# Optimization experiments

Hardware: AMD Instinct MI355X
Metric: run time of the kernel (lower is better)

Reference implementation:

```python
import jax, jax.numpy as jnp
import numpy as np

N, E, L, H, C, F, NCLASS, NGRAPH = 50000, 800000, 3, 2, 64, 128, 10, 64
NEG_SLOPE = 0.2


def setup_inputs() -> dict:
    key = jax.random.key(0)
    ks = jax.random.split(key, 8)
    x = jax.random.normal(ks[0], (N, F), dtype=jnp.float32)
    edge_index = jax.random.randint(ks[1], (2, E), 0, N, dtype=jnp.int64)
    batch = jnp.sort(jax.random.randint(ks[2], (N,), 0, NGRAPH, dtype=jnp.int64))
    s = 1.0 / np.sqrt(F)
    W = jax.random.normal(ks[3], (L, F, H * C), dtype=jnp.float32) * s
    att_src = jax.random.normal(ks[4], (L, H, C), dtype=jnp.float32) * s
    att_dst = jax.random.normal(ks[5], (L, H, C), dtype=jnp.float32) * s
    bias = jnp.zeros((L, H * C), dtype=jnp.float32)
    lin_w = jax.random.normal(ks[6], (H * C, NCLASS), dtype=jnp.float32) * s
    lin_b = jnp.zeros((NCLASS,), dtype=jnp.float32)
    return {"x": x, "edge_index": edge_index, "batch": batch, "W": W,
            "att_src": att_src, "att_dst": att_dst, "bias": bias,
            "lin_w": lin_w, "lin_b": lin_b}


def _gat_layer(x, src, dst, w, a_s, a_d, b):
    n = x.shape[0]
    h = (x @ w).reshape(n, H, C)                      # [N,H,C]
    alpha_src = jnp.sum(h * a_s, axis=-1)             # [N,H]
    alpha_dst = jnp.sum(h * a_d, axis=-1)             # [N,H]
    e = jax.nn.leaky_relu(alpha_src[src] + alpha_dst[dst], NEG_SLOPE)  # [E2,H]
    # scatter-softmax over incoming edges of each destination node
    m = jax.ops.segment_max(e, dst, num_segments=n)
    p = jnp.exp(e - m[dst])
    z = jax.ops.segment_sum(p, dst, num_segments=n)
    alpha = p / z[dst]                                # [E2,H]
    msg = h[src] * alpha[:, :, None]                  # [E2,H,C]
    out = jax.ops.segment_sum(msg, dst, num_segments=n)  # [N,H,C]
    return out.reshape(n, H * C) + b


def reference(x, edge_index, batch, W, att_src, att_dst, bias, lin_w, lin_b):
    n = x.shape[0]
    # PyG GATConv default: add self-loops
    loop = jnp.arange(n, dtype=edge_index.dtype)
    src = jnp.concatenate([edge_index[0], loop])
    dst = jnp.concatenate([edge_index[1], loop])
    for l in range(L):
        x = _gat_layer(x, src, dst, W[l], att_src[l], att_dst[l], bias[l])
        x = jax.nn.elu(x)  # activation; dropout/bn inactive (eval, use_bn=False)
    # global mean pool per graph
    sums = jax.ops.segment_sum(x, batch, num_segments=NGRAPH)
    cnt = jax.ops.segment_sum(jnp.ones((n,), x.dtype), batch, num_segments=NGRAPH)
    pooled = sums / jnp.maximum(cnt, 1.0)[:, None]    # [NGRAPH, H*C]
    logits = pooled @ lin_w + lin_b
    return jax.nn.softmax(logits, axis=1)
```

## Files before the change

### kernel.cpp

```cpp
#include <hip/hip_runtime.h>
#include <math.h>

#define NNODES 50000
#define NEDGES 800000
#define NLAYERS 3
#define NHEADS 2
#define NCH 64
#define FDIM 128
#define NCLS 10
#define NGRAPH 64
#define NEG_SLOPE 0.2f
#define NBLK ((NNODES + 255) / 256)
#define GEMMB ((NNODES + 63) / 64)
#define HISTB ((NEDGES + 255) / 256)

#define WAVE_SYNC()                      \
  do {                                   \
    __builtin_amdgcn_wave_barrier();     \
    __asm__ volatile("" ::: "memory");   \
  } while (0)

typedef __attribute__((ext_vector_type(8))) short bf16x8;
typedef __attribute__((ext_vector_type(4))) float f32x4;

__device__ __forceinline__ unsigned short f2bf(float f) {
  unsigned int u = __builtin_bit_cast(unsigned int, f);
  unsigned int r = u + 0x7FFFu + ((u >> 16) & 1u);
  return (unsigned short)(r >> 16);
}
__device__ __forceinline__ float bflo(unsigned v) {
  return __builtin_bit_cast(float, v << 16);
}
__device__ __forceinline__ float bfhi(unsigned v) {
  return __builtin_bit_cast(float, v & 0xFFFF0000u);
}

__global__ __launch_bounds__(256) void k_wprep(const float* __restrict__ W,
                                               unsigned* __restrict__ Wt) {
  __shared__ float Lt[128][132];
  int l = blockIdx.x;
  const float* Wl = W + (size_t)l * FDIM * FDIM;
  unsigned* Wtl = Wt + (size_t)l * FDIM * FDIM / 2;
  int t = threadIdx.x;
#pragma unroll
  for (int i = 0; i < 16; ++i) {
    int k = (t >> 5) + 8 * i;
    int n4 = (t & 31) * 4;
    float4 v = *(const float4*)(Wl + (size_t)k * 128 + n4);
    Lt[k][n4 + 0] = v.x;
    Lt[k][n4 + 1] = v.y;
    Lt[k][n4 + 2] = v.z;
    Lt[k][n4 + 3] = v.w;
  }
  __syncthreads();
  int n = t >> 1;
  int kh = (t & 1) * 64;
  for (int kk = 0; kk < 64; kk += 2) {
    unsigned pk = (unsigned)f2bf(Lt[kh + kk][n]) |
                  ((unsigned)f2bf(Lt[kh + kk + 1][n]) << 16);
    Wtl[n * 64 + (kh >> 1) + (kk >> 1)] = pk;
  }
}


__global__ __launch_bounds__(256) void k_scan1(const int* __restrict__ deg,
                                               int* __restrict__ pre,
                                               int* __restrict__ bsum) {
  __shared__ int ps[256];
  int t = threadIdx.x;
  int i = blockIdx.x * 256 + t;
  int c = (i < NNODES) ? (deg[i] + 1) : 0;
  ps[t] = c;
  __syncthreads();
  for (int off = 1; off < 256; off <<= 1) {
    int v = (t >= off) ? ps[t - off] : 0;
    __syncthreads();
    ps[t] += v;
    __syncthreads();
  }
  if (i < NNODES) pre[i] = ps[t] - c;
  if (t == 255) bsum[blockIdx.x] = ps[255];
}

__global__ __launch_bounds__(256) void k_scan2(const int* __restrict__ bsum,
                                               int* __restrict__ boff) {
  __shared__ int ps[256];
  int t = threadIdx.x;
  int c = (t < NBLK) ? bsum[t] : 0;
  ps[t] = c;
  __syncthreads();
  for (int off = 1; off < 256; off <<= 1) {
    int v = (t >= off) ? ps[t - off] : 0;
    __syncthreads();
    ps[t] += v;
    __syncthreads();
  }
  if (t < NBLK) boff[t] = ps[t] - c;
}

__global__ void k_scan3(const int* __restrict__ pre,
                        const int* __restrict__ boff,
                        int* __restrict__ row_ptr, int* __restrict__ csr) {
  int i = blockIdx.x * 256 + threadIdx.x;
  if (i < NNODES) {
    int o = pre[i] + boff[i >> 8];
    row_ptr[i] = o;
    csr[o] = i;
  }
  if (i == 0) row_ptr[NNODES] = NEDGES + NNODES;
}

__global__ void k_scatter(const int* __restrict__ ei,
                          const int* __restrict__ row_ptr,
                          const int* __restrict__ rank, int* __restrict__ csr) {
  int e = blockIdx.x * 256 + threadIdx.x;
  if (e < NEDGES) {
    int d = ei[NEDGES + e];
    csr[row_ptr[d] + 1 + rank[e]] = ei[e];
  }
}

__device__ __forceinline__ void gemm_body(int blk, const float* __restrict__ X,
                                          const unsigned* __restrict__ Wt,
                                          const float* __restrict__ a_sL,
                                          const float* __restrict__ a_dL,
                                          unsigned* __restrict__ Hb,
                                          float* __restrict__ as_,
                                          float* __restrict__ ad_) {
  __shared__ unsigned short Xs[64][136];
  __shared__ unsigned short Wsh[128][136];
  int t = threadIdx.x;
  int lane = t & 63;
  int w = t >> 6;
  int row0 = blk * 64;

  {
    int r = t >> 2;
    int gr = row0 + r;
    const float* xp = X + (size_t)gr * 128;
#pragma unroll
    for (int i = 0; i < 8; ++i) {
      int c4 = ((t & 3) + 4 * i) * 4;
      float4 v = make_float4(0.f, 0.f, 0.f, 0.f);
      if (gr < NNODES) v = *(const float4*)(xp + c4);
      unsigned lo = (unsigned)f2bf(v.x) | ((unsigned)f2bf(v.y) << 16);
      unsigned hi = (unsigned)f2bf(v.z) | ((unsigned)f2bf(v.w) << 16);
      *(uint2*)&Xs[r][c4] = make_uint2(lo, hi);
    }
  }
  {
    int n = t >> 1;
    const uint4* wp = (const uint4*)(Wt + n * 64 + (t & 1) * 32);
    int kh = (t & 1) * 64;
#pragma unroll
    for (int i = 0; i < 8; ++i) {
      uint4 v = wp[i];
      *(uint4*)&Wsh[n][kh + i * 8] = v;
    }
  }
  __syncthreads();

  int n16 = lane & 15;
  int quad = lane >> 4;
  int m0 = w * 16;
  f32x4 acc[8];
#pragma unroll
  for (int nt = 0; nt < 8; ++nt) {
    f32x4 z = {0.f, 0.f, 0.f, 0.f};
    acc[nt] = z;
  }
#pragma unroll
  for (int kk = 0; kk < 4; ++kk) {
    bf16x8 af = *(const bf16x8*)&Xs[m0 + n16][kk * 32 + quad * 8];
#pragma unroll
    for (int nt = 0; nt < 8; ++nt) {
      bf16x8 bf = *(const bf16x8*)&Wsh[nt * 16 + n16][kk * 32 + quad * 8];
      acc[nt] =
          __builtin_amdgcn_mfma_f32_16x16x32_bf16(af, bf, acc[nt], 0, 0, 0);
    }
  }

  float asv[8], adv[8];
#pragma unroll
  for (int nt = 0; nt < 8; ++nt) {
    asv[nt] = a_sL[nt * 16 + n16];
    adv[nt] = a_dL[nt * 16 + n16];
  }
#pragma unroll
  for (int r = 0; r < 4; ++r) {
    int row = row0 + m0 + quad * 4 + r;
    bool ok = (row < NNODES);
    float ps0 = 0.f, pd0 = 0.f, ps1 = 0.f, pd1 = 0.f;
#pragma unroll
    for (int nt = 0; nt < 4; ++nt) {
      ps0 += acc[nt][r] * asv[nt];
      pd0 += acc[nt][r] * adv[nt];
      ps1 += acc[nt + 4][r] * asv[nt + 4];
      pd1 += acc[nt + 4][r] * adv[nt + 4];
    }
#pragma unroll
    for (int off = 1; off < 16; off <<= 1) {
      ps0 += __shfl_xor(ps0, off, 64);
      pd0 += __shfl_xor(pd0, off, 64);
      ps1 += __shfl_xor(ps1, off, 64);
      pd1 += __shfl_xor(pd1, off, 64);
    }
    if (ok && n16 == 0) {
      as_[row * 2 + 0] = ps0;
      as_[row * 2 + 1] = ps1;
      ad_[row * 2 + 0] = pd0;
      ad_[row * 2 + 1] = pd1;
    }
    if (ok) {
#pragma unroll
      for (int nt = 0; nt < 4; ++nt) {
        unsigned pk = (unsigned)f2bf(acc[nt][r]) |
                      ((unsigned)f2bf(acc[nt + 4][r]) << 16);
        Hb[(size_t)row * 64 + nt * 16 + n16] = pk;
      }
    }
  }
}

__global__ __launch_bounds__(256) void k_gemm(const float* __restrict__ X,
                                              const unsigned* __restrict__ Wt,
                                              const float* __restrict__ a_sL,
                                              const float* __restrict__ a_dL,
                                              unsigned* __restrict__ Hb,
                                              float* __restrict__ as_,
                                              float* __restrict__ ad_) {
  gemm_body(blockIdx.x, X, Wt, a_sL, a_dL, Hb, as_, ad_);
}

__global__ __launch_bounds__(256) void k_front(
    const float* __restrict__ X, const unsigned* __restrict__ Wt,
    const float* __restrict__ a_sL, const float* __restrict__ a_dL,
    unsigned* __restrict__ Hb, float* __restrict__ as_,
    float* __restrict__ ad_, const int* __restrict__ ei, int* __restrict__ deg,
    int* __restrict__ rank, const int* __restrict__ batch,
    float* __restrict__ gcnt) {
  int b = blockIdx.x;
  if (b < GEMMB) {
    gemm_body(b, X, Wt, a_sL, a_dL, Hb, as_, ad_);
  } else if (b < GEMMB + HISTB) {
    int e = (b - GEMMB) * 256 + threadIdx.x;
    if (e < NEDGES) rank[e] = atomicAdd(&deg[ei[NEDGES + e]], 1);
  } else {
    __shared__ float loc[NGRAPH];
    int t = threadIdx.x;
    if (t < NGRAPH) loc[t] = 0.f;
    __syncthreads();
    int n = (b - GEMMB - HISTB) * 256 + t;
    if (n < NNODES) atomicAdd(&loc[batch[n]], 1.f);
    __syncthreads();
    if (t < NGRAPH && loc[t] > 0.f) atomicAdd(&gcnt[t], loc[t]);
  }
}

__global__ __launch_bounds__(256) void k_aggregate(
    const unsigned* __restrict__ Hb, const float* __restrict__ as_,
    const float* __restrict__ ad_, const int* __restrict__ row_ptr,
    const int* __restrict__ csr, const float* __restrict__ bias,
    float* __restrict__ Xout) {
  __shared__ float2 wb[4][64];
  __shared__ int sb[4][64];
  int wv = threadIdx.x >> 6;
  int lane = threadIdx.x & 63;
  int node = blockIdx.x * 4 + wv;
  if (node >= NNODES) return;
  int rs = row_ptr[node], re = row_ptr[node + 1];
  float2 adv = *(const float2*)&ad_[node * 2];
  const unsigned* Hl = Hb + lane;

  float z0 = 0.f, z1 = 0.f, acc0 = 0.f, acc1 = 0.f;
  for (int base = rs; base < re; base += 64) {
    int j = base + lane;
    float p0 = 0.f, p1 = 0.f;
    int s = 0;
    if (j < re) {
      s = csr[j];
      float2 asv = *(const float2*)&as_[s * 2];
      float e0 = asv.x + adv.x; e0 = (e0 > 0.f) ? e0 : NEG_SLOPE * e0;
      float e1 = asv.y + adv.y; e1 = (e1 > 0.f) ? e1 : NEG_SLOPE * e1;
      p0 = __expf(e0);
      p1 = __expf(e1);
    }
    z0 += p0;
    z1 += p1;
    wb[wv][lane] = make_float2(p0, p1);
    sb[wv][lane] = s;
    WAVE_SYNC();
    int cl = min(64, re - base);
    int jj = 0;
    for (; jj + 8 <= cl; jj += 8) {
      unsigned v0 = Hl[(size_t)sb[wv][jj + 0] * 64];
      unsigned v1 = Hl[(size_t)sb[wv][jj + 1] * 64];
      unsigned v2 = Hl[(size_t)sb[wv][jj + 2] * 64];
      unsigned v3 = Hl[(size_t)sb[wv][jj + 3] * 64];
      unsigned v4 = Hl[(size_t)sb[wv][jj + 4] * 64];
      unsigned v5 = Hl[(size_t)sb[wv][jj + 5] * 64];
      unsigned v6 = Hl[(size_t)sb[wv][jj + 6] * 64];
      unsigned v7 = Hl[(size_t)sb[wv][jj + 7] * 64];
      float2 w0 = wb[wv][jj + 0], w1 = wb[wv][jj + 1];
      float2 w2 = wb[wv][jj + 2], w3 = wb[wv][jj + 3];
      float2 w4 = wb[wv][jj + 4], w5 = wb[wv][jj + 5];
      float2 w6 = wb[wv][jj + 6], w7 = wb[wv][jj + 7];
      acc0 += w0.x * bflo(v0); acc1 += w0.y * bfhi(v0);
      acc0 += w1.x * bflo(v1); acc1 += w1.y * bfhi(v1);
      acc0 += w2.x * bflo(v2); acc1 += w2.y * bfhi(v2);
      acc0 += w3.x * bflo(v3); acc1 += w3.y * bfhi(v3);
      acc0 += w4.x * bflo(v4); acc1 += w4.y * bfhi(v4);
      acc0 += w5.x * bflo(v5); acc1 += w5.y * bfhi(v5);
      acc0 += w6.x * bflo(v6); acc1 += w6.y * bfhi(v6);
      acc0 += w7.x * bflo(v7); acc1 += w7.y * bfhi(v7);
    }
    for (; jj < cl; ++jj) {
      unsigned v = Hl[(size_t)sb[wv][jj] * 64];
      float2 w = wb[wv][jj];
      acc0 += w.x * bflo(v);
      acc1 += w.y * bfhi(v);
    }
    WAVE_SYNC();
  }
#pragma unroll
  for (int off = 32; off > 0; off >>= 1) {
    z0 += __shfl_xor(z0, off, 64);
    z1 += __shfl_xor(z1, off, 64);
  }
  float o0 = acc0 / z0 + bias[lane];
  float o1 = acc1 / z1 + bias[64 + lane];
  o0 = (o0 > 0.f) ? o0 : expm1f(o0);
  o1 = (o1 > 0.f) ? o1 : expm1f(o1);
  Xout[(size_t)node * 128 + lane] = o0;
  Xout[(size_t)node * 128 + 64 + lane] = o1;
}


__global__ __launch_bounds__(128) void k_pool(const float* __restrict__ Xf,
                                              const int* __restrict__ batch,
                                              float* __restrict__ gsum) {
  int c = threadIdx.x;
  int n0 = blockIdx.x * 64;
  if (n0 >= NNODES) return;
  int n1 = min(n0 + 64, NNODES);
  int cur = batch[n0];
  float acc = 0.f;
  for (int n = n0; n < n1; ++n) {
    int g = batch[n];
    if (g != cur) {
      atomicAdd(&gsum[cur * FDIM + c], acc);
      acc = 0.f;
      cur = g;
    }
    acc += Xf[(size_t)n * 128 + c];
  }
  atomicAdd(&gsum[cur * FDIM + c], acc);
}

__global__ __launch_bounds__(64) void k_final(const float* __restrict__ gsum,
                                              const float* __restrict__ gcnt,
                                              const float* __restrict__ lw,
                                              const float* __restrict__ lb,
                                              float* __restrict__ out) {
  int g = threadIdx.x;
  float inv = 1.f / fmaxf(gcnt[g], 1.f);
  float lg[NCLS];
#pragma unroll
  for (int k = 0; k < NCLS; ++k) lg[k] = lb[k];
  for (int c = 0; c < FDIM; ++c) {
    float pv = gsum[g * FDIM + c] * inv;
#pragma unroll
    for (int k = 0; k < NCLS; ++k) lg[k] += pv * lw[c * NCLS + k];
  }
  float mx = lg[0];
#pragma unroll
  for (int k = 1; k < NCLS; ++k) mx = fmaxf(mx, lg[k]);
  float s = 0.f;
#pragma unroll
  for (int k = 0; k < NCLS; ++k) {
    lg[k] = expf(lg[k] - mx);
    s += lg[k];
  }
  float invs = 1.f / s;
#pragma unroll
  for (int k = 0; k < NCLS; ++k) out[g * NCLS + k] = lg[k] * invs;
}


extern "C" void kernel_launch(void* const* d_in, const int* in_sizes, int n_in,
                              void* d_out, int out_size, void* d_ws,
                              size_t ws_size, hipStream_t stream) {
  const float* x = (const float*)d_in[0];
  const int* ei = (const int*)d_in[1];
  const int* batch = (const int*)d_in[2];
  const float* W = (const float*)d_in[3];
  const float* a_s = (const float*)d_in[4];
  const float* a_d = (const float*)d_in[5];
  const float* bias = (const float*)d_in[6];
  const float* lw = (const float*)d_in[7];
  const float* lb = (const float*)d_in[8];
  float* out = (float*)d_out;

  unsigned* Hb = (unsigned*)d_ws;
  float* xb = (float*)(Hb + (size_t)NNODES * 64);
  float* as_ = xb + (size_t)NNODES * 128;
  float* ad_ = as_ + (size_t)NNODES * 2;
  float* gsum = ad_ + (size_t)NNODES * 2;
  float* gcnt = gsum + NGRAPH * FDIM;
  int* deg = (int*)(gcnt + NGRAPH);
  int* row_ptr = deg + NNODES;
  int* csr = row_ptr + (NNODES + 1);
  int* pre = csr + (NEDGES + NNODES);
  int* bsum = pre + NNODES;
  int* boff = bsum + NBLK;
  int* rank = boff + NBLK;
  unsigned* Wt = (unsigned*)(rank + NEDGES);

  hipMemsetAsync(gsum, 0, (NGRAPH * FDIM + NGRAPH + NNODES) * 4, stream);
  k_wprep<<<NLAYERS, 256, 0, stream>>>(W, Wt);
  k_front<<<GEMMB + HISTB + NBLK, 256, 0, stream>>>(
      x, Wt, a_s, a_d, Hb, as_, ad_, ei, deg, rank, batch, gcnt);
  k_scan1<<<NBLK, 256, 0, stream>>>(deg, pre, bsum);
  k_scan2<<<1, 256, 0, stream>>>(bsum, boff);
  k_scan3<<<NBLK, 256, 0, stream>>>(pre, boff, row_ptr, csr);
  k_scatter<<<HISTB, 256, 0, stream>>>(ei, row_ptr, rank, csr);

  for (int l = 0; l < NLAYERS; ++l) {
    if (l > 0) {
      k_gemm<<<GEMMB, 256, 0, stream>>>(xb, Wt + (size_t)l * FDIM * FDIM / 2,
                                        a_s + l * FDIM, a_d + l * FDIM, Hb,
                                        as_, ad_);
    }
    k_aggregate<<<(NNODES + 3) / 4, 256, 0, stream>>>(
        Hb, as_, ad_, row_ptr, csr, bias + l * FDIM, xb);
  }
  k_pool<<<(NNODES + 63) / 64, 128, 0, stream>>>(xb, batch, gsum);
  k_final<<<1, 64, 0, stream>>>(gsum, gcnt, lw, lb, out);
}
```

Measured before the change: 334.6 us.

## Build CSR via two-pass bucketed radix sort and drop LDS staging in GEMM

Replaces the global per-edge atomic histogram, node-level scan and random scatter with a bucketed counting sort. Edges are first binned by destination into 128-node buckets using block-local LDS histograms. A bucket-major scan and partition pass follows, then a per-bucket pass that computes degrees, row pointers and CSR slots with shared-memory atomics. This is meant to cut contended global atomics and scattered writes. Separately, the GEMM now reads X and Wt directly from global memory into MFMA operands instead of staging through LDS, which trades shared-memory traffic and a barrier for redundant global/L2 reads of W.

Result: faster. 323.1 us (-3.4%).

```diff
diff --git a/kernel.cpp b/kernel.cpp
--- a/kernel.cpp
+++ b/kernel.cpp
@@ -12,7 +12,10 @@
 #define NEG_SLOPE 0.2f
 #define NBLK ((NNODES + 255) / 256)
 #define GEMMB ((NNODES + 63) / 64)
-#define HISTB ((NEDGES + 255) / 256)
+#define NB 391
+#define RADB 391
+#define SCN (NB * RADB)
+#define NS1 ((SCN + 511) / 512)
 
 #define WAVE_SYNC()                      \
   do {                                   \
@@ -62,64 +65,6 @@
   }
 }
 
-
-__global__ __launch_bounds__(256) void k_scan1(const int* __restrict__ deg,
-                                               int* __restrict__ pre,
-                                               int* __restrict__ bsum) {
-  __shared__ int ps[256];
-  int t = threadIdx.x;
-  int i = blockIdx.x * 256 + t;
-  int c = (i < NNODES) ? (deg[i] + 1) : 0;
-  ps[t] = c;
-  __syncthreads();
-  for (int off = 1; off < 256; off <<= 1) {
-    int v = (t >= off) ? ps[t - off] : 0;
-    __syncthreads();
-    ps[t] += v;
-    __syncthreads();
-  }
-  if (i < NNODES) pre[i] = ps[t] - c;
-  if (t == 255) bsum[blockIdx.x] = ps[255];
-}
-
-__global__ __launch_bounds__(256) void k_scan2(const int* __restrict__ bsum,
-                                               int* __restrict__ boff) {
-  __shared__ int ps[256];
-  int t = threadIdx.x;
-  int c = (t < NBLK) ? bsum[t] : 0;
-  ps[t] = c;
-  __syncthreads();
-  for (int off = 1; off < 256; off <<= 1) {
-    int v = (t >= off) ? ps[t - off] : 0;
-    __syncthreads();
-    ps[t] += v;
-    __syncthreads();
-  }
-  if (t < NBLK) boff[t] = ps[t] - c;
-}
-
-__global__ void k_scan3(const int* __restrict__ pre,
-                        const int* __restrict__ boff,
-                        int* __restrict__ row_ptr, int* __restrict__ csr) {
-  int i = blockIdx.x * 256 + threadIdx.x;
-  if (i < NNODES) {
-    int o = pre[i] + boff[i >> 8];
-    row_ptr[i] = o;
-    csr[o] = i;
-  }
-  if (i == 0) row_ptr[NNODES] = NEDGES + NNODES;
-}
-
-__global__ void k_scatter(const int* __restrict__ ei,
-                          const int* __restrict__ row_ptr,
-                          const int* __restrict__ rank, int* __restrict__ csr) {
-  int e = blockIdx.x * 256 + threadIdx.x;
-  if (e < NEDGES) {
-    int d = ei[NEDGES + e];
-    csr[row_ptr[d] + 1 + rank[e]] = ei[e];
-  }
-}
-
 __device__ __forceinline__ void gemm_body(int blk, const float* __restrict__ X,
                                           const unsigned* __restrict__ Wt,
                                           const float* __restrict__ a_sL,
@@ -127,42 +72,17 @@
                                           unsigned* __restrict__ Hb,
                                           float* __restrict__ as_,
                                           float* __restrict__ ad_) {
-  __shared__ unsigned short Xs[64][136];
-  __shared__ unsigned short Wsh[128][136];
   int t = threadIdx.x;
   int lane = t & 63;
   int w = t >> 6;
   int row0 = blk * 64;
-
-  {
-    int r = t >> 2;
-    int gr = row0 + r;
-    const float* xp = X + (size_t)gr * 128;
-#pragma unroll
-    for (int i = 0; i < 8; ++i) {
-      int c4 = ((t & 3) + 4 * i) * 4;
-      float4 v = make_float4(0.f, 0.f, 0.f, 0.f);
-      if (gr < NNODES) v = *(const float4*)(xp + c4);
-      unsigned lo = (unsigned)f2bf(v.x) | ((unsigned)f2bf(v.y) << 16);
-      unsigned hi = (unsigned)f2bf(v.z) | ((unsigned)f2bf(v.w) << 16);
-      *(uint2*)&Xs[r][c4] = make_uint2(lo, hi);
-    }
-  }
-  {
-    int n = t >> 1;
-    const uint4* wp = (const uint4*)(Wt + n * 64 + (t & 1) * 32);
-    int kh = (t & 1) * 64;
-#pragma unroll
-    for (int i = 0; i < 8; ++i) {
-      uint4 v = wp[i];
-      *(uint4*)&Wsh[n][kh + i * 8] = v;
-    }
-  }
-  __syncthreads();
-
   int n16 = lane & 15;
   int quad = lane >> 4;
   int m0 = w * 16;
+
+  int gr = row0 + m0 + n16;
+  const float* xp = X + (size_t)min(gr, NNODES - 1) * 128;
+
   f32x4 acc[8];
 #pragma unroll
   for (int nt = 0; nt < 8; ++nt) {
@@ -171,10 +91,17 @@
   }
 #pragma unroll
   for (int kk = 0; kk < 4; ++kk) {
-    bf16x8 af = *(const bf16x8*)&Xs[m0 + n16][kk * 32 + quad * 8];
+    float4 va = *(const float4*)(xp + kk * 32 + quad * 8);
+    float4 vb = *(const float4*)(xp + kk * 32 + quad * 8 + 4);
+    bf16x8 af;
+    af[0] = (short)f2bf(va.x); af[1] = (short)f2bf(va.y);
+    af[2] = (short)f2bf(va.z); af[3] = (short)f2bf(va.w);
+    af[4] = (short)f2bf(vb.x); af[5] = (short)f2bf(vb.y);
+    af[6] = (short)f2bf(vb.z); af[7] = (short)f2bf(vb.w);
 #pragma unroll
     for (int nt = 0; nt < 8; ++nt) {
-      bf16x8 bf = *(const bf16x8*)&Wsh[nt * 16 + n16][kk * 32 + quad * 8];
+      bf16x8 bf = *(const bf16x8*)(Wt + (size_t)(nt * 16 + n16) * 64 +
+                                   kk * 16 + quad * 4);
       acc[nt] =
           __builtin_amdgcn_mfma_f32_16x16x32_bf16(af, bf, acc[nt], 0, 0, 0);
     }
@@ -236,24 +163,144 @@
     const float* __restrict__ X, const unsigned* __restrict__ Wt,
     const float* __restrict__ a_sL, const float* __restrict__ a_dL,
     unsigned* __restrict__ Hb, float* __restrict__ as_,
-    float* __restrict__ ad_, const int* __restrict__ ei, int* __restrict__ deg,
-    int* __restrict__ rank, const int* __restrict__ batch,
-    float* __restrict__ gcnt) {
+    float* __restrict__ ad_, const int* __restrict__ ei, int* __restrict__ bh,
+    const int* __restrict__ batch, float* __restrict__ gcnt) {
   int b = blockIdx.x;
   if (b < GEMMB) {
     gemm_body(b, X, Wt, a_sL, a_dL, Hb, as_, ad_);
-  } else if (b < GEMMB + HISTB) {
-    int e = (b - GEMMB) * 256 + threadIdx.x;
-    if (e < NEDGES) rank[e] = atomicAdd(&deg[ei[NEDGES + e]], 1);
+  } else if (b < GEMMB + RADB) {
+    __shared__ int hist[NB];
+    int blk = b - GEMMB;
+    int t = threadIdx.x;
+    for (int i = t; i < NB; i += 256) hist[i] = 0;
+    __syncthreads();
+    int e0 = blk * 2048;
+#pragma unroll
+    for (int i = 0; i < 8; ++i) {
+      int e = e0 + i * 256 + t;
+      if (e < NEDGES) atomicAdd(&hist[ei[NEDGES + e] >> 7], 1);
+    }
+    __syncthreads();
+    for (int i = t; i < NB; i += 256) bh[i * RADB + blk] = hist[i];
   } else {
     __shared__ float loc[NGRAPH];
     int t = threadIdx.x;
     if (t < NGRAPH) loc[t] = 0.f;
     __syncthreads();
-    int n = (b - GEMMB - HISTB) * 256 + t;
+    int n = (b - GEMMB - RADB) * 256 + t;
     if (n < NNODES) atomicAdd(&loc[batch[n]], 1.f);
     __syncthreads();
     if (t < NGRAPH && loc[t] > 0.f) atomicAdd(&gcnt[t], loc[t]);
+  }
+}
+
+__global__ __launch_bounds__(256) void k_s1(int* __restrict__ sc,
+                                            int* __restrict__ bpart) {
+  __shared__ int ps[256];
+  int t = threadIdx.x;
+  int f0 = blockIdx.x * 512 + 2 * t;
+  int x0 = (f0 < SCN) ? sc[f0] : 0;
+  int x1 = (f0 + 1 < SCN) ? sc[f0 + 1] : 0;
+  int pair = x0 + x1;
+  ps[t] = pair;
+  __syncthreads();
+  for (int off = 1; off < 256; off <<= 1) {
+    int v = (t >= off) ? ps[t - off] : 0;
+    __syncthreads();
+    ps[t] += v;
+    __syncthreads();
+  }
+  int ex = ps[t] - pair;
+  if (f0 < SCN) sc[f0] = ex;
+  if (f0 + 1 < SCN) sc[f0 + 1] = ex + x0;
+  if (t == 255) bpart[blockIdx.x] = ps[255];
+}
+
+__global__ __launch_bounds__(256) void k_s2(int* __restrict__ bpart) {
+  __shared__ int ps[256];
+  int t = threadIdx.x;
+  int x0 = (2 * t < NS1) ? bpart[2 * t] : 0;
+  int x1 = (2 * t + 1 < NS1) ? bpart[2 * t + 1] : 0;
+  int pair = x0 + x1;
+  ps[t] = pair;
+  __syncthreads();
+  for (int off = 1; off < 256; off <<= 1) {
+    int v = (t >= off) ? ps[t - off] : 0;
+    __syncthreads();
+    ps[t] += v;
+    __syncthreads();
+  }
+  int ex = ps[t] - pair;
+  if (2 * t < NS1) bpart[2 * t] = ex;
+  if (2 * t + 1 < NS1) bpart[2 * t + 1] = ex + x0;
+}
+
+__global__ __launch_bounds__(256) void k_s3(int* __restrict__ sc,
+                                            const int* __restrict__ bpart) {
+  int t = threadIdx.x;
+  int f0 = blockIdx.x * 512 + 2 * t;
+  int add = bpart[blockIdx.x];
+  if (f0 < SCN) sc[f0] += add;
+  if (f0 + 1 < SCN) sc[f0 + 1] += add;
+}
+
+__global__ __launch_bounds__(256) void k_passB(const int* __restrict__ ei,
+                                               const int* __restrict__ sc,
+                                               unsigned* __restrict__ ebuf) {
+  __shared__ int curs[NB];
+  int blk = blockIdx.x, t = threadIdx.x;
+  for (int i = t; i < NB; i += 256) curs[i] = sc[i * RADB + blk];
+  __syncthreads();
+  int e0 = blk * 2048;
+#pragma unroll
+  for (int i = 0; i < 8; ++i) {
+    int e = e0 + i * 256 + t;
+    if (e < NEDGES) {
+      int s = ei[e];
+      int d = ei[NEDGES + e];
+      int pos = atomicAdd(&curs[d >> 7], 1);
+      ebuf[pos] = ((unsigned)s << 7) | (unsigned)(d & 127);
+    }
+  }
+}
+
+__global__ __launch_bounds__(256) void k_passC(const unsigned* __restrict__ ebuf,
+                                               const int* __restrict__ sc,
+                                               int* __restrict__ row_ptr,
+                                               int* __restrict__ csr) {
+  __shared__ int deg[128];
+  __shared__ int scn[128];
+  int b = blockIdx.x, t = threadIdx.x;
+  int node0 = b * 128;
+  int nn = min(128, NNODES - node0);
+  int estart = sc[b * RADB];
+  int eend = (b + 1 < NB) ? sc[(b + 1) * RADB] : NEDGES;
+  if (t < 128) deg[t] = 0;
+  __syncthreads();
+  for (int e = estart + t; e < eend; e += 256)
+    atomicAdd(&deg[ebuf[e] & 127], 1);
+  __syncthreads();
+  if (t < 128) scn[t] = (t < nn) ? deg[t] + 1 : 0;
+  __syncthreads();
+  for (int off = 1; off < 128; off <<= 1) {
+    int v = (t < 128 && t >= off) ? scn[t - off] : 0;
+    __syncthreads();
+    if (t < 128) scn[t] += v;
+    __syncthreads();
+  }
+  int base = estart + node0;
+  if (t < nn) {
+    int st = base + (t ? scn[t - 1] : 0);
+    row_ptr[node0 + t] = st;
+    csr[st] = node0 + t;
+    deg[t] = st + 1;
+  }
+  if (b == 0 && t == 0) row_ptr[NNODES] = NEDGES + NNODES;
+  __syncthreads();
+  for (int e = estart + t; e < eend; e += 256) {
+    unsigned v = ebuf[e];
+    int pos = atomicAdd(&deg[v & 127], 1);
+    csr[pos] = (int)(v >> 7);
   }
 }
 
@@ -407,23 +454,22 @@
   float* ad_ = as_ + (size_t)NNODES * 2;
   float* gsum = ad_ + (size_t)NNODES * 2;
   float* gcnt = gsum + NGRAPH * FDIM;
-  int* deg = (int*)(gcnt + NGRAPH);
-  int* row_ptr = deg + NNODES;
+  int* row_ptr = (int*)(gcnt + NGRAPH);
   int* csr = row_ptr + (NNODES + 1);
-  int* pre = csr + (NEDGES + NNODES);
-  int* bsum = pre + NNODES;
-  int* boff = bsum + NBLK;
-  int* rank = boff + NBLK;
-  unsigned* Wt = (unsigned*)(rank + NEDGES);
-
-  hipMemsetAsync(gsum, 0, (NGRAPH * FDIM + NGRAPH + NNODES) * 4, stream);
+  int* sc = csr + (NEDGES + NNODES);
+  int* bpart = sc + SCN;
+  unsigned* ebuf = (unsigned*)(bpart + NS1);
+  unsigned* Wt = ebuf + (NEDGES + 1024);
+
+  hipMemsetAsync(gsum, 0, (NGRAPH * FDIM + NGRAPH) * 4, stream);
   k_wprep<<<NLAYERS, 256, 0, stream>>>(W, Wt);
-  k_front<<<GEMMB + HISTB + NBLK, 256, 0, stream>>>(
-      x, Wt, a_s, a_d, Hb, as_, ad_, ei, deg, rank, batch, gcnt);
-  k_scan1<<<NBLK, 256, 0, stream>>>(deg, pre, bsum);
-  k_scan2<<<1, 256, 0, stream>>>(bsum, boff);
-  k_scan3<<<NBLK, 256, 0, stream>>>(pre, boff, row_ptr, csr);
-  k_scatter<<<HISTB, 256, 0, stream>>>(ei, row_ptr, rank, csr);
+  k_front<<<GEMMB + RADB + NBLK, 256, 0, stream>>>(
+      x, Wt, a_s, a_d, Hb, as_, ad_, ei, sc, batch, gcnt);
+  k_s1<<<NS1, 256, 0, stream>>>(sc, bpart);
+  k_s2<<<1, 256, 0, stream>>>(bpart);
+  k_s3<<<NS1, 256, 0, stream>>>(sc, bpart);
+  k_passB<<<RADB, 256, 0, stream>>>(ei, sc, ebuf);
+  k_passC<<<NB, 256, 0, stream>>>(ebuf, sc, row_ptr, csr);
 
   for (int l = 0; l < NLAYERS; ++l) {
     if (l > 0) {
```
